# Optimization experiments

Measured on AMD Instinct MI355X. Metric: run time of the kernel, lower is better.

The kernel has to match this reference:

```python
import jax, jax.numpy as jnp
import numpy as np

N = 100000      # nodes
E = 1600000     # edges (avg degree 16)
IN_FEATS = 128
HEADS = 4
OUT_FEATS = 16
NEG_SLOPE = 0.2
EPS = 1e-16


def setup_inputs() -> dict:
    key = jax.random.key(0)
    k1, k2, k3, k4, k5, k6 = jax.random.split(key, 6)
    feat = jax.random.normal(k1, (N, IN_FEATS), dtype=jnp.float32)
    # xavier-ish scale for params
    W = jax.random.normal(k2, (IN_FEATS, HEADS * OUT_FEATS), dtype=jnp.float32) * 0.1
    attn_l = jax.random.normal(k3, (1, HEADS, OUT_FEATS), dtype=jnp.float32) * 0.1
    attn_r = jax.random.normal(k4, (1, HEADS, OUT_FEATS), dtype=jnp.float32) * 0.1
    src_index = jax.random.randint(k5, (E,), 0, N, dtype=jnp.int32)
    trg_index = jax.random.randint(k6, (E,), 0, N, dtype=jnp.int32)
    return {"feat": feat, "W": W, "attn_l": attn_l, "attn_r": attn_r,
            "src_index": src_index, "trg_index": trg_index}


def reference(feat, W, attn_l, attn_r, src_index, trg_index):
    # dropout layers are identity in eval mode
    n = feat.shape[0]
    h = (feat @ W).reshape(n, HEADS, OUT_FEATS)            # [N,H,F]
    el = jnp.sum(h * attn_l, axis=-1)                      # [N,H]
    er = jnp.sum(h * attn_r, axis=-1)                      # [N,H]
    s = el[src_index] + er[trg_index]                      # [E,H] edge scores
    s = jnp.where(s > 0, s, NEG_SLOPE * s)                 # LeakyReLU(0.2)
    # neighborhood-aware softmax over incoming edges of each target node
    s = s - jnp.max(s)                                     # global max shift (as in source)
    e = jnp.exp(s)                                         # [E,H]
    denom = jax.ops.segment_sum(e, trg_index, num_segments=n)  # [N,H]
    attn = e / (denom[trg_index] + EPS)                    # [E,H]
    # weighted aggregation of lifted source features into target nodes
    msg = h[src_index] * attn[:, :, None]                  # [E,H,F]
    h_prime = jax.ops.segment_sum(msg, trg_index, num_segments=n)  # [N,H,F]
    return h_prime.reshape(n, HEADS * OUT_FEATS)
```

## Files before the change

### kernel.cpp

```cpp
#include <hip/hip_runtime.h>

typedef unsigned short ushort_t;
typedef __attribute__((ext_vector_type(8))) short bf16x8;
typedef __attribute__((ext_vector_type(4))) float f32x4v;

static __device__ __forceinline__ float bf2f(ushort_t u) {
  union { unsigned int i; float f; } v; v.i = ((unsigned int)u) << 16; return v.f;
}
static __device__ __forceinline__ ushort_t f2bf(float f) {
  union { float f; unsigned int i; } v; v.f = f;
  unsigned int r = v.i + 0x7FFFu + ((v.i >> 16) & 1u);
  return (ushort_t)(r >> 16);
}
static __device__ __forceinline__ float leaky(float s) {
  return s > 0.f ? s : 0.2f * s;
}

__global__ __launch_bounds__(256) void packw_hist(
    const float* __restrict__ W, const float* __restrict__ attnl,
    const float* __restrict__ attnr, ushort_t* __restrict__ wfrag,
    const int* __restrict__ trg, int E, int nbkt,
    int* __restrict__ blockHist, int nb3, int epb)
{
  const int b = blockIdx.x;
  const int t = threadIdx.x;
  if (b == nb3) {
    const int kc = t >> 6, l = t & 63;
    const int q = l >> 4, n = l & 15;
    #pragma unroll
    for (int tile = 0; tile < 5; ++tile) {
      #pragma unroll
      for (int j = 0; j < 8; ++j) {
        const int k = kc * 32 + q * 8 + j;
        float v = 0.f;
        if (tile < 4) {
          v = W[k * 64 + tile * 16 + n];
        } else if (n < 4) {
          for (int f = 0; f < 16; ++f)
            v += W[k * 64 + n * 16 + f] * attnl[n * 16 + f];
        } else if (n < 8) {
          const int hd = n - 4;
          for (int f = 0; f < 16; ++f)
            v += W[k * 64 + hd * 16 + f] * attnr[hd * 16 + f];
        }
        wfrag[((tile * 4 + kc) * 64 + l) * 8 + j] = f2bf(v);
      }
    }
    return;
  }
  __shared__ int hist[256];
  hist[t] = 0;
  __syncthreads();
  const int start = b * epb;
  const int end = min(start + epb, E);
  for (int e = start + t; e < end; e += 256)
    atomicAdd(&hist[trg[e] >> 9], 1);
  __syncthreads();
  if (t < nbkt) blockHist[b * nbkt + t] = hist[t];
}

__global__ __launch_bounds__(64) void bucket_scan(
    int* __restrict__ blockHist, int nb3, int nbkt, int* __restrict__ colTotal)
{
  const int b = blockIdx.x;
  const int l = threadIdx.x;
  int carry = 0;
  for (int r = 0; r * 64 < nb3; ++r) {
    const int i = r * 64 + l;
    int v = (i < nb3) ? blockHist[i * nbkt + b] : 0;
    int incl = v;
    #pragma unroll
    for (int d = 1; d < 64; d <<= 1) {
      int u = __shfl_up(incl, d, 64);
      if (l >= d) incl += u;
    }
    if (i < nb3) blockHist[i * nbkt + b] = carry + incl - v;
    carry += __shfl(incl, 63, 64);
  }
  if (l == 0) colTotal[b] = carry;
}

__global__ __launch_bounds__(64) void bucket_base(
    const int* __restrict__ colTotal, int nbkt, int* __restrict__ bucketBase,
    int* __restrict__ rowoff, int N, int E)
{
  const int l = threadIdx.x;
  int carry = 0;
  for (int r = 0; r * 64 < nbkt; ++r) {
    const int i = r * 64 + l;
    int v = (i < nbkt) ? colTotal[i] : 0;
    int incl = v;
    #pragma unroll
    for (int d = 1; d < 64; d <<= 1) {
      int u = __shfl_up(incl, d, 64);
      if (l >= d) incl += u;
    }
    if (i < nbkt) bucketBase[i] = carry + incl - v;
    carry += __shfl(incl, 63, 64);
  }
  if (l == 0) { bucketBase[nbkt] = carry; rowoff[N] = E; }
}

__global__ __launch_bounds__(256) void bucket_scatter(
    const int* __restrict__ src, const int* __restrict__ trg, int E, int nbkt,
    const int* __restrict__ blockHist, const int* __restrict__ bucketBase,
    unsigned int* __restrict__ binned, int epb)
{
  __shared__ int cursor[256];
  const int t = threadIdx.x, b = blockIdx.x;
  if (t < nbkt) cursor[t] = bucketBase[t] + blockHist[b * nbkt + t];
  __syncthreads();
  const int start = b * epb;
  const int end = min(start + epb, E);
  for (int e = start + t; e < end; e += 256) {
    const int ti = trg[e];
    const int bkt = ti >> 9;
    const int pos = atomicAdd(&cursor[bkt], 1);
    binned[pos] = ((unsigned int)src[e] << 9) | (unsigned int)(ti & 511);
  }
}

__global__ __launch_bounds__(256) void gat_linear(
    const float* __restrict__ feat, const ushort_t* __restrict__ wfrag,
    ushort_t* __restrict__ h_out, float* __restrict__ el, float* __restrict__ er,
    float* __restrict__ blockmax2, int N)
{
  __shared__ ushort_t sFb[64 * 136];
  __shared__ float wmax[8];
  const int t = threadIdx.x;
  const int b = blockIdx.x;
  const int w = t >> 6, l = t & 63;
  const int q = l >> 4, m = l & 15;

  const float4* gF = (const float4*)(feat + (size_t)b * 64 * 128);
  #pragma unroll
  for (int i = 0; i < 8; ++i) {
    const int idx = i * 256 + t;
    const int node = idx >> 5, off = idx & 31;
    float4 v = make_float4(0.f, 0.f, 0.f, 0.f);
    if (b * 64 + node < N) v = gF[idx];
    unsigned int p0 = ((unsigned int)f2bf(v.y) << 16) | f2bf(v.x);
    unsigned int p1 = ((unsigned int)f2bf(v.w) << 16) | f2bf(v.z);
    *(uint2*)(sFb + node * 136 + off * 4) = make_uint2(p0, p1);
  }
  __syncthreads();

  bf16x8 a[4];
  const ushort_t* arow = sFb + (w * 16 + m) * 136 + q * 8;
  #pragma unroll
  for (int kc = 0; kc < 4; ++kc)
    a[kc] = *(const bf16x8*)(arow + kc * 32);

  #pragma unroll
  for (int tile = 0; tile < 4; ++tile) {
    f32x4v acc = {0.f, 0.f, 0.f, 0.f};
    #pragma unroll
    for (int kc = 0; kc < 4; ++kc) {
      bf16x8 bfr = *(const bf16x8*)(wfrag + ((tile * 4 + kc) * 64 + l) * 8);
      acc = __builtin_amdgcn_mfma_f32_16x16x32_bf16(a[kc], bfr, acc, 0, 0, 0);
    }
    #pragma unroll
    for (int r = 0; r < 4; ++r) {
      const int gn = b * 64 + w * 16 + q * 4 + r;
      if (gn < N) h_out[(size_t)gn * 64 + tile * 16 + m] = f2bf(acc[r]);
    }
  }

  f32x4v acc4 = {0.f, 0.f, 0.f, 0.f};
  #pragma unroll
  for (int kc = 0; kc < 4; ++kc) {
    bf16x8 bfr = *(const bf16x8*)(wfrag + ((4 * 4 + kc) * 64 + l) * 8);
    acc4 = __builtin_amdgcn_mfma_f32_16x16x32_bf16(a[kc], bfr, acc4, 0, 0, 0);
  }
  float mel = -1e30f, mer = -1e30f;
  #pragma unroll
  for (int r = 0; r < 4; ++r) {
    const int gn = b * 64 + w * 16 + q * 4 + r;
    const float v = acc4[r];
    if (m < 4) {
      if (gn < N) el[gn * 4 + m] = v;
      mel = fmaxf(mel, v);
    } else if (m < 8) {
      if (gn < N) er[gn * 4 + (m - 4)] = v;
      mer = fmaxf(mer, v);
    }
  }
  #pragma unroll
  for (int o = 1; o <= 32; o <<= 1) {
    mel = fmaxf(mel, __shfl_xor(mel, o, 64));
    mer = fmaxf(mer, __shfl_xor(mer, o, 64));
  }
  if (l == 0) { wmax[w * 2] = mel; wmax[w * 2 + 1] = mer; }
  __syncthreads();
  if (t == 0) {
    float aa = fmaxf(fmaxf(wmax[0], wmax[2]), fmaxf(wmax[4], wmax[6]));
    float cc = fmaxf(fmaxf(wmax[1], wmax[3]), fmaxf(wmax[5], wmax[7]));
    blockmax2[b * 2] = aa;
    blockmax2[b * 2 + 1] = cc;
  }
}

__global__ __launch_bounds__(512) void fine_scatter(
    const unsigned int* __restrict__ binned, const int* __restrict__ bucketBase,
    int* __restrict__ rowoff, int* __restrict__ csrsrc, int N,
    const float* __restrict__ blockmax2, int nbL, float* __restrict__ gmaxM)
{
  __shared__ int cnt[512];
  __shared__ int ws[8];
  __shared__ float wmg[16];
  const int t = threadIdx.x, b = blockIdx.x;
  const int l = t & 63, w = t >> 6;
  const int base = bucketBase[b];
  const int end = bucketBase[b + 1];
  cnt[t] = 0;
  if (b == 0) {
    float mel = -1e30f, mer = -1e30f;
    for (int i = t; i < nbL; i += 512) {
      mel = fmaxf(mel, blockmax2[i * 2]);
      mer = fmaxf(mer, blockmax2[i * 2 + 1]);
    }
    #pragma unroll
    for (int o = 1; o <= 32; o <<= 1) {
      mel = fmaxf(mel, __shfl_xor(mel, o, 64));
      mer = fmaxf(mer, __shfl_xor(mer, o, 64));
    }
    if (l == 0) { wmg[w * 2] = mel; wmg[w * 2 + 1] = mer; }
  }
  __syncthreads();
  if (b == 0 && t == 0) {
    float aa = -1e30f, cc = -1e30f;
    for (int i = 0; i < 8; ++i) {
      aa = fmaxf(aa, wmg[i * 2]);
      cc = fmaxf(cc, wmg[i * 2 + 1]);
    }
    gmaxM[0] = fmaxf(0.f, aa + cc);
  }
  for (int i = base + t; i < end; i += 512)
    atomicAdd(&cnt[binned[i] & 511u], 1);
  __syncthreads();
  const int v = cnt[t];
  int incl = v;
  #pragma unroll
  for (int d = 1; d < 64; d <<= 1) {
    int u = __shfl_up(incl, d, 64);
    if (l >= d) incl += u;
  }
  if (l == 63) ws[w] = incl;
  __syncthreads();
  int woff = 0;
  for (int i = 0; i < w; ++i) woff += ws[i];
  const int loc = woff + incl - v;
  cnt[t] = loc;
  const int gt = b * 512 + t;
  if (gt < N) rowoff[gt] = base + loc;
  __syncthreads();
  for (int i = base + t; i < end; i += 512) {
    const unsigned int pv = binned[i];
    const int lt = (int)(pv & 511u);
    const int pos = base + atomicAdd(&cnt[lt], 1);
    csrsrc[pos] = (int)(pv >> 9);
  }
}

#define UNPACK_FMA(hv, p, acc) do { \
  union { unsigned int i; float f; } c_; \
  c_.i = (hv).x << 16;          acc[0] += c_.f * (p); \
  c_.i = (hv).x & 0xffff0000u;  acc[1] += c_.f * (p); \
  c_.i = (hv).y << 16;          acc[2] += c_.f * (p); \
  c_.i = (hv).y & 0xffff0000u;  acc[3] += c_.f * (p); \
  c_.i = (hv).z << 16;          acc[4] += c_.f * (p); \
  c_.i = (hv).z & 0xffff0000u;  acc[5] += c_.f * (p); \
  c_.i = (hv).w << 16;          acc[6] += c_.f * (p); \
  c_.i = (hv).w & 0xffff0000u;  acc[7] += c_.f * (p); \
} while (0)

__global__ __launch_bounds__(256) void gat_agg(
    const int* __restrict__ csrsrc, const int* __restrict__ rowoff,
    const float4* __restrict__ el4, const float4* __restrict__ er4,
    const ushort_t* __restrict__ hbf, const float* __restrict__ gmaxM,
    float* __restrict__ out, int N)
{
  __shared__ float sP[4 * 64 * 4];
  __shared__ int sS[4 * 64];
  const int t = threadIdx.x;
  const int l = t & 63;
  const int w = t >> 6;
  const int nbase = blockIdx.x * 16 + w * 4;
  const int rg = l >> 3;
  const int cg = l & 7;
  const int hd2 = cg >> 1;
  const int ks = l >> 4;
  const int le = l & 15;
  const float M = gmaxM[0];
  float* sPw = sP + w * 256;
  int* sSw = sS + w * 64;
  const ushort_t* hcg = hbf + cg * 8;

  const int nk = nbase + ks;
  const int rs = rowoff[min(nk, N)];
  const int re = rowoff[min(nk + 1, N)];
  const float4 ernk = (rs < re) ? er4[nk]
                                : make_float4(0.f, 0.f, 0.f, 0.f);
  int deg = re - rs;
  deg = max(deg, __shfl_xor(deg, 16, 64));
  deg = max(deg, __shfl_xor(deg, 32, 64));
  const int chunks = (deg + 15) >> 4;

  float aA[8] = {0.f,0.f,0.f,0.f,0.f,0.f,0.f,0.f};
  float aB[8] = {0.f,0.f,0.f,0.f,0.f,0.f,0.f,0.f};
  float dA = 0.f, dB = 0.f;

  for (int c = 0; c < chunks; ++c) {
    int sn = 0;
    float4 pv = make_float4(0.f, 0.f, 0.f, 0.f);
    const int ei = rs + c * 16 + le;
    if (ei < re) {
      sn = csrsrc[ei];
      const float4 a = el4[sn];
      pv.x = __expf(leaky(a.x + ernk.x) - M);
      pv.y = __expf(leaky(a.y + ernk.y) - M);
      pv.z = __expf(leaky(a.z + ernk.z) - M);
      pv.w = __expf(leaky(a.w + ernk.w) - M);
    }
    *(float4*)(sPw + l * 4) = pv;
    sSw[l] = sn;

    const int rem = min(deg - c * 16, 16);
    const int jmax = (rem + 3) >> 2;
    for (int j = 0; j < jmax; ++j) {
      const int iA = ((rg >> 2) * 16) + (rg & 3) + j * 4;
      const int iB = iA + 32;
      const int sA = sSw[iA];
      const int sB = sSw[iB];
      const float pA = sPw[iA * 4 + hd2];
      const float pB = sPw[iB * 4 + hd2];
      const uint4 hA = *(const uint4*)(hcg + (size_t)sA * 64);
      const uint4 hB = *(const uint4*)(hcg + (size_t)sB * 64);
      UNPACK_FMA(hA, pA, aA);
      UNPACK_FMA(hB, pB, aB);
      dA += pA;
      dB += pB;
    }
  }

  #pragma unroll
  for (int o = 8; o <= 16; o <<= 1) {
    #pragma unroll
    for (int i = 0; i < 8; ++i) {
      aA[i] += __shfl_xor(aA[i], o, 64);
      aB[i] += __shfl_xor(aB[i], o, 64);
    }
    dA += __shfl_xor(dA, o, 64);
    dB += __shfl_xor(dB, o, 64);
  }
  if ((rg & 3) == 0) {
    const int nA = nbase + (rg >> 2);
    const int nB = nA + 2;
    const float rA = 1.0f / (dA + 1e-16f);
    const float rB = 1.0f / (dB + 1e-16f);
    if (nA < N) {
      float4* orow = (float4*)(out + (size_t)nA * 64 + cg * 8);
      orow[0] = make_float4(aA[0] * rA, aA[1] * rA, aA[2] * rA, aA[3] * rA);
      orow[1] = make_float4(aA[4] * rA, aA[5] * rA, aA[6] * rA, aA[7] * rA);
    }
    if (nB < N) {
      float4* orow = (float4*)(out + (size_t)nB * 64 + cg * 8);
      orow[0] = make_float4(aB[0] * rB, aB[1] * rB, aB[2] * rB, aB[3] * rB);
      orow[1] = make_float4(aB[4] * rB, aB[5] * rB, aB[6] * rB, aB[7] * rB);
    }
  }
}

extern "C" void kernel_launch(void* const* d_in, const int* in_sizes, int n_in,
                              void* d_out, int out_size, void* d_ws, size_t ws_size,
                              hipStream_t stream) {
  const float* feat  = (const float*)d_in[0];
  const float* W     = (const float*)d_in[1];
  const float* attnl = (const float*)d_in[2];
  const float* attnr = (const float*)d_in[3];
  const int* src = (const int*)d_in[4];
  const int* trg = (const int*)d_in[5];
  float* out = (float*)d_out;

  const int N = in_sizes[0] / 128;
  const int E = in_sizes[4];

  const int nbL  = (N + 63) / 64;
  const int nbkt = (N + 511) >> 9;

  char* p = (char*)d_ws;
  auto take = [&](size_t bytes) -> char* {
    char* r = p;
    p += (bytes + 255) & ~(size_t)255;
    return r;
  };
  ushort_t* h_bf  = (ushort_t*)take((size_t)N * 64 * 2);
  float* el       = (float*)take((size_t)N * 16);
  float* er       = (float*)take((size_t)N * 16);
  int* rowoff     = (int*)take((size_t)(N + 1) * 4);
  int* csrsrc     = (int*)take((size_t)E * 4);
  unsigned int* binned = (unsigned int*)take((size_t)E * 4);
  ushort_t* wfrag = (ushort_t*)take(5 * 4 * 64 * 8 * 2);
  int* colTotal   = (int*)take((size_t)nbkt * 4);
  int* bucketBase = (int*)take((size_t)(nbkt + 1) * 4);
  float* blockmax2 = (float*)take((size_t)nbL * 2 * 4);
  float* gmaxM    = (float*)take(256);

  const size_t used = (size_t)(p - (char*)d_ws);
  const size_t avail = (ws_size > used + 512) ? (ws_size - used - 512) : 0;
  int nb3 = (int)(avail / ((size_t)nbkt * 4));
  if (nb3 > 800) nb3 = 800;
  if (nb3 < 64) nb3 = 64;
  int epb = (E + nb3 - 1) / nb3;
  nb3 = (E + epb - 1) / epb;
  int* blockHist  = (int*)take((size_t)nb3 * nbkt * 4);

  packw_hist<<<nb3 + 1, 256, 0, stream>>>(W, attnl, attnr, wfrag,
                                          trg, E, nbkt, blockHist, nb3, epb);
  bucket_scan<<<nbkt, 64, 0, stream>>>(blockHist, nb3, nbkt, colTotal);
  bucket_base<<<1, 64, 0, stream>>>(colTotal, nbkt, bucketBase, rowoff, N, E);
  bucket_scatter<<<nb3, 256, 0, stream>>>(src, trg, E, nbkt, blockHist,
                                          bucketBase, binned, epb);
  gat_linear<<<nbL, 256, 0, stream>>>(feat, wfrag, h_bf, el, er,
                                      blockmax2, N);
  fine_scatter<<<nbkt, 512, 0, stream>>>(binned, bucketBase, rowoff, csrsrc,
                                         N, blockmax2, nbL, gmaxM);
  gat_agg<<<(N + 15) / 16, 256, 0, stream>>>(csrsrc, rowoff, (const float4*)el,
                                             (const float4*)er, h_bf,
                                             gmaxM, out, N);
}
```

Baseline: 202.5 us.

## Replace two-level bucket sort CSR build with global-atomic degree count and scan

Replaces the two-pass bucketed counting sort (per-block bucket histograms, bucket scan, coarse scatter, then per-bucket fine scatter in shared memory) with a direct CSR build. Per-node degrees come from global atomics, a three-kernel prefix scan produces the row offsets, and a scatter kernel uses global atomic cursors. This removes the intermediate binned array and its extra read/write pass, at the cost of 2×E global atomics to random addresses instead of shared-memory atomics. Because the cursor atomics run in arbitrary order, the order of neighbours within each row becomes nondeterministic. The global-max reduction moves into its own small kernel, and a memset is added.

```diff
diff --git a/kernel.cpp b/kernel.cpp
--- a/kernel.cpp
+++ b/kernel.cpp
@@ -4,9 +4,6 @@
 typedef __attribute__((ext_vector_type(8))) short bf16x8;
 typedef __attribute__((ext_vector_type(4))) float f32x4v;
 
-static __device__ __forceinline__ float bf2f(ushort_t u) {
-  union { unsigned int i; float f; } v; v.i = ((unsigned int)u) << 16; return v.f;
-}
 static __device__ __forceinline__ ushort_t f2bf(float f) {
   union { float f; unsigned int i; } v; v.f = f;
   unsigned int r = v.i + 0x7FFFu + ((v.i >> 16) & 1u);
@@ -16,11 +13,11 @@
   return s > 0.f ? s : 0.2f * s;
 }
 
-__global__ __launch_bounds__(256) void packw_hist(
+__global__ __launch_bounds__(256) void packw_deg(
     const float* __restrict__ W, const float* __restrict__ attnl,
     const float* __restrict__ attnr, ushort_t* __restrict__ wfrag,
-    const int* __restrict__ trg, int E, int nbkt,
-    int* __restrict__ blockHist, int nb3, int epb)
+    const int* __restrict__ trg, int E, int* __restrict__ deg,
+    int nb3, int epb)
 {
   const int b = blockIdx.x;
   const int t = threadIdx.x;
@@ -48,75 +45,93 @@
     }
     return;
   }
-  __shared__ int hist[256];
-  hist[t] = 0;
-  __syncthreads();
   const int start = b * epb;
   const int end = min(start + epb, E);
   for (int e = start + t; e < end; e += 256)
-    atomicAdd(&hist[trg[e] >> 9], 1);
+    atomicAdd(&deg[trg[e]], 1);
+}
+
+__global__ __launch_bounds__(256) void scan_part(
+    const int* __restrict__ deg, int n, int* __restrict__ partial)
+{
+  __shared__ int wtot[4];
+  const int t = threadIdx.x, b = blockIdx.x;
+  const int l = t & 63, w = t >> 6;
+  const int base = b * 1024 + t * 4;
+  int s = 0;
+  #pragma unroll
+  for (int j = 0; j < 4; ++j)
+    if (base + j < n) s += deg[base + j];
+  #pragma unroll
+  for (int o = 1; o <= 32; o <<= 1) s += __shfl_xor(s, o, 64);
+  if (l == 0) wtot[w] = s;
   __syncthreads();
-  if (t < nbkt) blockHist[b * nbkt + t] = hist[t];
-}
-
-__global__ __launch_bounds__(64) void bucket_scan(
-    int* __restrict__ blockHist, int nb3, int nbkt, int* __restrict__ colTotal)
-{
-  const int b = blockIdx.x;
+  if (t == 0) partial[b] = wtot[0] + wtot[1] + wtot[2] + wtot[3];
+}
+
+__global__ __launch_bounds__(64) void scan_mid(
+    int* __restrict__ partial, int nsb)
+{
   const int l = threadIdx.x;
   int carry = 0;
-  for (int r = 0; r * 64 < nb3; ++r) {
+  for (int r = 0; r * 64 < nsb; ++r) {
     const int i = r * 64 + l;
-    int v = (i < nb3) ? blockHist[i * nbkt + b] : 0;
+    int v = (i < nsb) ? partial[i] : 0;
     int incl = v;
     #pragma unroll
     for (int d = 1; d < 64; d <<= 1) {
       int u = __shfl_up(incl, d, 64);
       if (l >= d) incl += u;
     }
-    if (i < nb3) blockHist[i * nbkt + b] = carry + incl - v;
+    if (i < nsb) partial[i] = carry + incl - v;
     carry += __shfl(incl, 63, 64);
   }
-  if (l == 0) colTotal[b] = carry;
-}
-
-__global__ __launch_bounds__(64) void bucket_base(
-    const int* __restrict__ colTotal, int nbkt, int* __restrict__ bucketBase,
-    int* __restrict__ rowoff, int N, int E)
-{
-  const int l = threadIdx.x;
-  int carry = 0;
-  for (int r = 0; r * 64 < nbkt; ++r) {
-    const int i = r * 64 + l;
-    int v = (i < nbkt) ? colTotal[i] : 0;
-    int incl = v;
-    #pragma unroll
-    for (int d = 1; d < 64; d <<= 1) {
-      int u = __shfl_up(incl, d, 64);
-      if (l >= d) incl += u;
-    }
-    if (i < nbkt) bucketBase[i] = carry + incl - v;
-    carry += __shfl(incl, 63, 64);
-  }
-  if (l == 0) { bucketBase[nbkt] = carry; rowoff[N] = E; }
-}
-
-__global__ __launch_bounds__(256) void bucket_scatter(
-    const int* __restrict__ src, const int* __restrict__ trg, int E, int nbkt,
-    const int* __restrict__ blockHist, const int* __restrict__ bucketBase,
-    unsigned int* __restrict__ binned, int epb)
-{
-  __shared__ int cursor[256];
+}
+
+__global__ __launch_bounds__(256) void scan_fix(
+    const int* __restrict__ deg, int n, int E, const int* __restrict__ partial,
+    int* __restrict__ rowoff, int* __restrict__ cursor)
+{
+  __shared__ int wtot[4];
   const int t = threadIdx.x, b = blockIdx.x;
-  if (t < nbkt) cursor[t] = bucketBase[t] + blockHist[b * nbkt + t];
+  const int l = t & 63, w = t >> 6;
+  const int base = b * 1024 + t * 4;
+  int v0 = 0, v1 = 0, v2 = 0, v3 = 0;
+  if (base + 0 < n) v0 = deg[base + 0];
+  if (base + 1 < n) v1 = deg[base + 1];
+  if (base + 2 < n) v2 = deg[base + 2];
+  if (base + 3 < n) v3 = deg[base + 3];
+  const int e1 = v0, e2 = v0 + v1, e3 = e2 + v2;
+  const int tsum = e3 + v3;
+  int incl = tsum;
+  #pragma unroll
+  for (int d = 1; d < 64; d <<= 1) {
+    int u = __shfl_up(incl, d, 64);
+    if (l >= d) incl += u;
+  }
+  const int texcl = incl - tsum;
+  if (l == 63) wtot[w] = incl;
   __syncthreads();
+  int woff = 0;
+  for (int i = 0; i < w; ++i) woff += wtot[i];
+  const int tb = partial[b] + woff + texcl;
+  if (base + 0 < n) { rowoff[base + 0] = tb;      cursor[base + 0] = tb; }
+  if (base + 1 < n) { rowoff[base + 1] = tb + e1; cursor[base + 1] = tb + e1; }
+  if (base + 2 < n) { rowoff[base + 2] = tb + e2; cursor[base + 2] = tb + e2; }
+  if (base + 3 < n) { rowoff[base + 3] = tb + e3; cursor[base + 3] = tb + e3; }
+  if (b == 0 && t == 0) rowoff[n] = E;
+}
+
+__global__ __launch_bounds__(256) void csr_scatter(
+    const int* __restrict__ src, const int* __restrict__ trg, int E,
+    int* __restrict__ cursor, int* __restrict__ csrsrc, int nb3, int epb)
+{
+  const int t = threadIdx.x, b = blockIdx.x;
   const int start = b * epb;
   const int end = min(start + epb, E);
   for (int e = start + t; e < end; e += 256) {
-    const int ti = trg[e];
-    const int bkt = ti >> 9;
-    const int pos = atomicAdd(&cursor[bkt], 1);
-    binned[pos] = ((unsigned int)src[e] << 9) | (unsigned int)(ti & 511);
+    const int pos = atomicAdd(&cursor[trg[e]], 1);
+    csrsrc[pos] = src[e];
   }
 }
 
@@ -200,65 +215,27 @@
   }
 }
 
-__global__ __launch_bounds__(512) void fine_scatter(
-    const unsigned int* __restrict__ binned, const int* __restrict__ bucketBase,
-    int* __restrict__ rowoff, int* __restrict__ csrsrc, int N,
+__global__ __launch_bounds__(256) void gmax_reduce(
     const float* __restrict__ blockmax2, int nbL, float* __restrict__ gmaxM)
 {
-  __shared__ int cnt[512];
-  __shared__ int ws[8];
-  __shared__ float wmg[16];
-  const int t = threadIdx.x, b = blockIdx.x;
-  const int l = t & 63, w = t >> 6;
-  const int base = bucketBase[b];
-  const int end = bucketBase[b + 1];
-  cnt[t] = 0;
-  if (b == 0) {
-    float mel = -1e30f, mer = -1e30f;
-    for (int i = t; i < nbL; i += 512) {
-      mel = fmaxf(mel, blockmax2[i * 2]);
-      mer = fmaxf(mer, blockmax2[i * 2 + 1]);
-    }
-    #pragma unroll
-    for (int o = 1; o <= 32; o <<= 1) {
-      mel = fmaxf(mel, __shfl_xor(mel, o, 64));
-      mer = fmaxf(mer, __shfl_xor(mer, o, 64));
-    }
-    if (l == 0) { wmg[w * 2] = mel; wmg[w * 2 + 1] = mer; }
-  }
+  __shared__ float wmg[8];
+  const int t = threadIdx.x, l = t & 63, w = t >> 6;
+  float mel = -1e30f, mer = -1e30f;
+  for (int i = t; i < nbL; i += 256) {
+    mel = fmaxf(mel, blockmax2[i * 2]);
+    mer = fmaxf(mer, blockmax2[i * 2 + 1]);
+  }
+  #pragma unroll
+  for (int o = 1; o <= 32; o <<= 1) {
+    mel = fmaxf(mel, __shfl_xor(mel, o, 64));
+    mer = fmaxf(mer, __shfl_xor(mer, o, 64));
+  }
+  if (l == 0) { wmg[w * 2] = mel; wmg[w * 2 + 1] = mer; }
   __syncthreads();
-  if (b == 0 && t == 0) {
-    float aa = -1e30f, cc = -1e30f;
-    for (int i = 0; i < 8; ++i) {
-      aa = fmaxf(aa, wmg[i * 2]);
-      cc = fmaxf(cc, wmg[i * 2 + 1]);
-    }
+  if (t == 0) {
+    float aa = fmaxf(fmaxf(wmg[0], wmg[2]), fmaxf(wmg[4], wmg[6]));
+    float cc = fmaxf(fmaxf(wmg[1], wmg[3]), fmaxf(wmg[5], wmg[7]));
     gmaxM[0] = fmaxf(0.f, aa + cc);
-  }
-  for (int i = base + t; i < end; i += 512)
-    atomicAdd(&cnt[binned[i] & 511u], 1);
-  __syncthreads();
-  const int v = cnt[t];
-  int incl = v;
-  #pragma unroll
-  for (int d = 1; d < 64; d <<= 1) {
-    int u = __shfl_up(incl, d, 64);
-    if (l >= d) incl += u;
-  }
-  if (l == 63) ws[w] = incl;
-  __syncthreads();
-  int woff = 0;
-  for (int i = 0; i < w; ++i) woff += ws[i];
-  const int loc = woff + incl - v;
-  cnt[t] = loc;
-  const int gt = b * 512 + t;
-  if (gt < N) rowoff[gt] = base + loc;
-  __syncthreads();
-  for (int i = base + t; i < end; i += 512) {
-    const unsigned int pv = binned[i];
-    const int lt = (int)(pv & 511u);
-    const int pos = base + atomicAdd(&cnt[lt], 1);
-    csrsrc[pos] = (int)(pv >> 9);
   }
 }
 
@@ -385,8 +362,10 @@
   const int N = in_sizes[0] / 128;
   const int E = in_sizes[4];
 
-  const int nbL  = (N + 63) / 64;
-  const int nbkt = (N + 511) >> 9;
+  const int nbL = (N + 63) / 64;
+  const int nsb = (N + 1023) / 1024;
+  const int nb3 = 800;
+  const int epb = (E + nb3 - 1) / nb3;
 
   char* p = (char*)d_ws;
   auto take = [&](size_t bytes) -> char* {
@@ -399,32 +378,24 @@
   float* er       = (float*)take((size_t)N * 16);
   int* rowoff     = (int*)take((size_t)(N + 1) * 4);
   int* csrsrc     = (int*)take((size_t)E * 4);
-  unsigned int* binned = (unsigned int*)take((size_t)E * 4);
+  int* deg        = (int*)take((size_t)N * 4);
+  int* cursor     = (int*)take((size_t)N * 4);
+  int* partial    = (int*)take((size_t)(nsb + 1) * 4);
   ushort_t* wfrag = (ushort_t*)take(5 * 4 * 64 * 8 * 2);
-  int* colTotal   = (int*)take((size_t)nbkt * 4);
-  int* bucketBase = (int*)take((size_t)(nbkt + 1) * 4);
   float* blockmax2 = (float*)take((size_t)nbL * 2 * 4);
   float* gmaxM    = (float*)take(256);
 
-  const size_t used = (size_t)(p - (char*)d_ws);
-  const size_t avail = (ws_size > used + 512) ? (ws_size - used - 512) : 0;
-  int nb3 = (int)(avail / ((size_t)nbkt * 4));
-  if (nb3 > 800) nb3 = 800;
-  if (nb3 < 64) nb3 = 64;
-  int epb = (E + nb3 - 1) / nb3;
-  nb3 = (E + epb - 1) / epb;
-  int* blockHist  = (int*)take((size_t)nb3 * nbkt * 4);
-
-  packw_hist<<<nb3 + 1, 256, 0, stream>>>(W, attnl, attnr, wfrag,
-                                          trg, E, nbkt, blockHist, nb3, epb);
-  bucket_scan<<<nbkt, 64, 0, stream>>>(blockHist, nb3, nbkt, colTotal);
-  bucket_base<<<1, 64, 0, stream>>>(colTotal, nbkt, bucketBase, rowoff, N, E);
-  bucket_scatter<<<nb3, 256, 0, stream>>>(src, trg, E, nbkt, blockHist,
-                                          bucketBase, binned, epb);
+  hipMemsetAsync(deg, 0, (size_t)N * 4, stream);
+
+  packw_deg<<<nb3 + 1, 256, 0, stream>>>(W, attnl, attnr, wfrag,
+                                         trg, E, deg, nb3, epb);
+  scan_part<<<nsb, 256, 0, stream>>>(deg, N, partial);
+  scan_mid<<<1, 64, 0, stream>>>(partial, nsb);
+  scan_fix<<<nsb, 256, 0, stream>>>(deg, N, E, partial, rowoff, cursor);
+  csr_scatter<<<nb3, 256, 0, stream>>>(src, trg, E, cursor, csrsrc, nb3, epb);
   gat_linear<<<nbL, 256, 0, stream>>>(feat, wfrag, h_bf, el, er,
                                       blockmax2, N);
-  fine_scatter<<<nbkt, 512, 0, stream>>>(binned, bucketBase, rowoff, csrsrc,
-                                         N, blockmax2, nbL, gmaxM);
+  gmax_reduce<<<1, 256, 0, stream>>>(blockmax2, nbL, gmaxM);
   gat_agg<<<(N + 15) / 16, 256, 0, stream>>>(csrsrc, rowoff, (const float4*)el,
                                              (const float4*)er, h_bf,
                                              gmaxM, out, N);
```

Result: slower. 369.1 us (+82.2%).
